# Kernel optimization log

Measured on AMD Instinct MI355X. Metric: run time of the kernel, lower is better.

## Reference

```python
import jax, jax.numpy as jnp
import numpy as np

N_QUBITS = 6
N_LAYERS = 2
QSVT_DEGREE = 3
BATCH = 128
SEQ_LEN = 512
DIM = 2 ** N_QUBITS
# wire 0 is the most-significant bit in the statevector index (PennyLane convention)
_POP = np.array([bin(i).count('1') for i in range(DIM)], dtype=np.float32)
PHASE_SIGN = jnp.asarray(N_QUBITS - 2.0 * _POP)  # (DIM,): sum_w (1 - 2*bit_w)


def _rx(t):
    c = jnp.cos(0.5 * t).astype(jnp.complex64)
    s = (-1j * jnp.sin(0.5 * t)).astype(jnp.complex64)
    return jnp.stack([jnp.stack([c, s]), jnp.stack([s, c])])


def _ry(t):
    c = jnp.cos(0.5 * t).astype(jnp.complex64)
    s = jnp.sin(0.5 * t).astype(jnp.complex64)
    return jnp.stack([jnp.stack([c, -s]), jnp.stack([s, c])])


def _rz(t):
    e = jnp.exp(-0.5j * t.astype(jnp.complex64))
    z = jnp.zeros((), jnp.complex64)
    return jnp.stack([jnp.stack([e, z]), jnp.stack([z, jnp.conj(e)])])


def _apply_1q(psi, U, w):
    # psi: (B,) + (2,)*N_QUBITS ; U: (2,2) complex, same for all batch elems
    psi = jnp.moveaxis(psi, 1 + w, -1)
    psi = psi @ U.T
    return jnp.moveaxis(psi, -1, 1 + w)


def _apply_ry_batched(psi, theta, w):
    # RY with a per-batch angle theta: (B,)
    psi = jnp.moveaxis(psi, 1 + w, -1)
    c = jnp.cos(0.5 * theta).reshape((-1,) + (1,) * (N_QUBITS - 1))
    s = jnp.sin(0.5 * theta).reshape((-1,) + (1,) * (N_QUBITS - 1))
    a, b = psi[..., 0], psi[..., 1]
    psi = jnp.stack([c * a - s * b, s * a + c * b], axis=-1)
    return jnp.moveaxis(psi, -1, 1 + w)


def _cnot(psi, c, t):
    p0 = jax.lax.index_in_dim(psi, 0, axis=1 + c, keepdims=True)
    p1 = jax.lax.index_in_dim(psi, 1, axis=1 + c, keepdims=True)
    p1 = jnp.flip(p1, axis=1 + t)
    return jnp.concatenate([p0, p1], axis=1 + c)


def _circuit_step(h, x, params, poly):
    # h, x: (B, N_QUBITS) angles. Returns <Z_w> per qubit: (B, N_QUBITS).
    B = h.shape[0]
    # 1) state encoding: RY(h_w)|0> = cos(h/2)|0> + sin(h/2)|1>  (product state)
    c, s = jnp.cos(0.5 * h), jnp.sin(0.5 * h)
    psi = jnp.ones((B, 1), jnp.complex64)
    for w in range(N_QUBITS):
        amp = jnp.stack([c[:, w], s[:, w]], axis=-1).astype(jnp.complex64)  # (B,2)
        psi = (psi[:, :, None] * amp[:, None, :]).reshape(B, -1)
    psi = psi.reshape((B,) + (2,) * N_QUBITS)
    # 2) QSVT block: RZ(coeff*pi) on every wire fuses into one diagonal phase
    for d in range(QSVT_DEGREE + 1):
        theta = poly[d] * np.pi
        phase = jnp.exp((-0.5j) * theta * PHASE_SIGN)  # (DIM,)
        psi = (psi.reshape(B, -1) * phase[None, :]).reshape((B,) + (2,) * N_QUBITS)
        for i in range(N_QUBITS - 1):
            psi = _cnot(psi, i, i + 1)
        psi = _cnot(psi, N_QUBITS - 1, 0)  # ring closure
    # 3) variational layers: per-wire RZ@RY@RX (RX applied first), then CNOT chain
    idx = 0
    for _ in range(N_LAYERS):
        for i in range(N_QUBITS):
            U = _rz(params[idx + 2]) @ _ry(params[idx + 1]) @ _rx(params[idx])
            psi = _apply_1q(psi, U, i)
            idx += 3
        for i in range(N_QUBITS - 1):
            psi = _cnot(psi, i, i + 1)
    # 4) input injection: RY(x_w) with per-batch angles
    for w in range(N_QUBITS):
        psi = _apply_ry_batched(psi, x[:, w], w)
    # 5) measurement: <Z_w> = P(bit_w=0) - P(bit_w=1)
    p = jnp.abs(psi) ** 2
    zs = []
    for w in range(N_QUBITS):
        axes = tuple(a for a in range(1, N_QUBITS + 1) if a != 1 + w)
        pw = p.sum(axis=axes)  # (B,2)
        zs.append(pw[:, 0] - pw[:, 1])
    return jnp.stack(zs, axis=-1)


def _ssm_pass(angles, params, poly, reverse):
    a = jnp.flip(angles, axis=1) if reverse else angles
    xs = jnp.moveaxis(a, 1, 0)  # (T, B, n)
    h0 = jnp.zeros((a.shape[0], N_QUBITS), jnp.float32)

    def step(h, x):
        hn = _circuit_step(h, x, params, poly)
        return hn, hn

    _, ys = jax.lax.scan(step, h0, xs)
    out = jnp.moveaxis(ys, 0, 1)  # (B, T, n)
    return jnp.flip(out, axis=1) if reverse else out


def setup_inputs() -> dict:
    key = jax.random.key(0)
    k0, k1, k2, k3 = jax.random.split(key, 4)
    angles = jax.random.uniform(k0, (BATCH, SEQ_LEN, N_QUBITS), jnp.float32) * np.float32(np.pi)
    poly_coeffs = jax.random.normal(k1, (QSVT_DEGREE + 1,), jnp.float32) * 0.1
    fwd_params = jax.random.normal(k2, (N_QUBITS * N_LAYERS * 3,), jnp.float32) * 0.1
    bwd_params = jax.random.normal(k3, (N_QUBITS * N_LAYERS * 3,), jnp.float32) * 0.1
    fwd_coeff = jnp.full((1,), 0.5, jnp.float32)
    bwd_coeff = jnp.full((1,), 0.5, jnp.float32)
    return {'angles': angles, 'poly_coeffs': poly_coeffs, 'fwd_params': fwd_params,
            'bwd_params': bwd_params, 'fwd_coeff': fwd_coeff, 'bwd_coeff': bwd_coeff}


def reference(angles, poly_coeffs, fwd_params, bwd_params, fwd_coeff, bwd_coeff):
    h_fwd = _ssm_pass(angles, fwd_params, poly_coeffs, reverse=False)
    h_bwd = _ssm_pass(angles, bwd_params, poly_coeffs, reverse=True)
    return jax.nn.sigmoid(fwd_coeff) * h_fwd + jax.nn.sigmoid(bwd_coeff) * h_bwd
```

## Files before the change

### kernel.cpp

```cpp
#include <hip/hip_runtime.h>
#include <hip/hip_bf16.h>
#include <stdint.h>

#define BATCH 128
#define SEQ   512
#define NW    6
#define DIM   64
#define NELEM (BATCH * SEQ * NW)
#define PI_F  3.14159265358979323846f

typedef float v2f __attribute__((ext_vector_type(2)));

__device__ __forceinline__ v2f pkfma(float s, v2f m, v2f a) {
    return __builtin_elementwise_fma((v2f){s, s}, m, a);
}

template <int CTRL>
__device__ __forceinline__ void red_stage3(float v[3]) {
#pragma unroll
    for (int k = 0; k < 3; ++k)
        v[k] += __int_as_float(__builtin_amdgcn_update_dpp(
            0, __float_as_int(v[k]), CTRL, 0xF, 0xF, false));
}

__device__ __forceinline__ void sincos_half(float h, float& s, float& c) {
    const float u = h * h;
    c = fmaf(u, fmaf(u, fmaf(u, -2.1701389e-5f, 2.6041667e-3f), -0.125f), 1.0f);
    s = h * fmaf(u, fmaf(u, fmaf(u, -1.5501e-6f, 2.6041667e-4f), -2.0833333e-2f), 0.5f);
}

__global__ void k_detect(const uint32_t* __restrict__ a, int* __restrict__ flag) {
    __shared__ int cnt;
    if (threadIdx.x == 0) cnt = 0;
    __syncthreads();
    uint32_t w = a[threadIdx.x];
    uint32_t e = (w >> 8) & 0xFFu;
    if (e >= 0x3Au && e <= 0x41u) atomicAdd(&cnt, 1);
    __syncthreads();
    if (threadIdx.x == 0) *flag = (cnt >= 128) ? 1 : 0;
}

__device__ __forceinline__ float ldf(const void* p, int i, bool bf) {
    if (bf) {
        uint32_t u = (uint32_t)((const uint16_t*)p)[i];
        return __uint_as_float(u << 16);
    }
    return ((const float*)p)[i];
}

__global__ void k_convert(const void* ang, const void* poly, const void* fp,
                          const void* bp, const void* fc, const void* bc,
                          float* __restrict__ cs, float* __restrict__ misc,
                          const int* __restrict__ flag) {
    const bool bf = (*flag != 0);
    const int i = blockIdx.x * blockDim.x + threadIdx.x;
    if (i < NELEM) {
        float x = ldf(ang, i, bf);
        float s, c;
        __sincosf(x, &s, &c);
        cs[2 * i]     = c;
        cs[2 * i + 1] = s;
    }
    if (i < 4)                    misc[i]            = ldf(poly, i, bf);
    else if (i >= 64 && i < 100)  misc[4 + (i - 64)] = ldf(fp, i - 64, bf);
    else if (i >= 128 && i < 164) misc[40 + (i - 128)] = ldf(bp, i - 128, bf);
    else if (i == 200)            misc[76] = ldf(fc, 0, bf);
    else if (i == 201)            misc[77] = ldf(bc, 0, bf);
}

__global__ void __launch_bounds__(64) k_msetup(const float* __restrict__ misc,
                                               float* __restrict__ Mg) {
    const int p   = threadIdx.x;
    const int col = blockIdx.x & 63;
    const int dir = blockIdx.x >> 6;
    const float* poly = misc;
    const float* prm  = misc + (dir ? 40 : 4);

    float yr = (p == col) ? 1.f : 0.f;
    float yi = 0.f;

#pragma unroll
    for (int d = 0; d < 4; ++d) {
        const float th = 0.5f * PI_F * poly[d] *
                         (float)(6 - 2 * (int)__popc((unsigned)p));
        float s, c;
        __sincosf(th, &s, &c);
        const float nr = yr * c + yi * s;
        const float ni = yi * c - yr * s;
        yr = nr; yi = ni;
#pragma unroll
        for (int k = 0; k < 6; ++k) {
            const int cw = k, tw = (k + 1) % 6;
            const int src = p ^ (((p >> (5 - cw)) & 1) << (5 - tw));
            yr = __shfl(yr, src, 64);
            yi = __shfl(yi, src, 64);
        }
    }

    int idx = 0;
#pragma unroll
    for (int l = 0; l < 2; ++l) {
#pragma unroll
        for (int w = 0; w < 6; ++w) {
            float cx, sx, cy, sy, cz, sz;
            __sincosf(0.5f * prm[idx + 0], &sx, &cx);
            __sincosf(0.5f * prm[idx + 1], &sy, &cy);
            __sincosf(0.5f * prm[idx + 2], &sz, &cz);
            idx += 3;
            const float A = cy * cx, B = sy * sx, C = sy * cx, D = cy * sx;
            const float U00r = cz * A + sz * B, U00i = cz * B - sz * A;
            const float U11r = U00r,            U11i = sz * A - cz * B;
            const float Xr   = cz * C + sz * D, Xi   = sz * C - cz * D;
            const int m  = 1 << (5 - w);
            const int bb = (p >> (5 - w)) & 1;
            const float C1r = bb ? U11r : U00r;
            const float C1i = bb ? U11i : U00i;
            const float C2r = bb ? Xr : -Xr;
            const float C2i = Xi;
            const float pr = __shfl_xor(yr, m, 64);
            const float pi = __shfl_xor(yi, m, 64);
            const float nr = C1r * yr - C1i * yi + C2r * pr - C2i * pi;
            const float ni = C1r * yi + C1i * yr + C2r * pi + C2i * pr;
            yr = nr; yi = ni;
        }
#pragma unroll
        for (int k = 0; k < 5; ++k) {
            const int src = p ^ (((p >> (5 - k)) & 1) << (5 - (k + 1)));
            yr = __shfl(yr, src, 64);
            yi = __shfl(yi, src, 64);
        }
    }

    float* out = Mg + ((size_t)(dir * 64 + p) * 64 + (size_t)col) * 2;
    out[0] = yr;
    out[1] = yi;
}

__global__ void __launch_bounds__(256, 1) k_sim(const float* __restrict__ cs,
                                                const float* __restrict__ Mg,
                                                float* __restrict__ hbuf) {
    const int tid   = threadIdx.x;
    const int lane  = tid & 63;
    const int wv    = tid >> 6;
    const int chain = blockIdx.x;
    const int dir   = chain >> 7;
    const int b     = chain & 127;
    float* orow = hbuf + (size_t)dir * NELEM + (size_t)b * (SEQ * NW);
    const float* csrow = cs + (size_t)b * (SEQ * NW * 2);

    __shared__ __align__(16) float  cl[SEQ * 12];
    __shared__ __align__(16) float  zb[SEQ * NW];
    __shared__ float2 pY[2][4][DIM];
    __shared__ __align__(16) float  mR[12];

    {
        const float4* src = (const float4*)csrow;
        float4* dst = (float4*)cl;
#pragma unroll
        for (int k = 0; k < 6; ++k) {
            const int idx = tid + k * 256;
            dst[idx] = src[idx];
        }
    }

    v2f Mres[16];
    {
        const float2* mr2 =
            (const float2*)(Mg + (size_t)(dir * 64 + lane) * 128 + 32 * wv);
#pragma unroll
        for (int k = 0; k < 16; ++k) Mres[k] = (v2f){mr2[k].x, mr2[k].y};
    }

    const int w0  = (wv & 1) * 3;
    const int isX = wv >> 1;
    int zmask3[3], bpa3[3];
#pragma unroll
    for (int k = 0; k < 3; ++k) {
        const int w = w0 + k;
        zmask3[k] = ((lane >> (5 - w)) & 1) << 31;
        bpa3[k]   = (lane ^ (1 << (5 - w))) << 2;
    }

    float h[6] = {0.f, 0.f, 0.f, 0.f, 0.f, 0.f};

    auto encode_matvec = [&](v2f& acc) {
        float cw6[6], sw6[6];
#pragma unroll
        for (int w = 0; w < 6; ++w) sincos_half(h[w], sw6[w], cw6[w]);
        const float t0 = (wv & 2) ? sw6[0] : cw6[0];
        const float t1 = (wv & 1) ? sw6[1] : cw6[1];
        const float A  = t0 * t1;
        float GH[4], GL[4];
        GH[0] = cw6[2] * cw6[3]; GH[1] = cw6[2] * sw6[3];
        GH[2] = sw6[2] * cw6[3]; GH[3] = sw6[2] * sw6[3];
#pragma unroll
        for (int a = 0; a < 4; ++a) GH[a] *= A;
        GL[0] = cw6[4] * cw6[5]; GL[1] = cw6[4] * sw6[5];
        GL[2] = sw6[4] * cw6[5]; GL[3] = sw6[4] * sw6[5];
        v2f y = {0.f, 0.f};
#pragma unroll
        for (int a = 0; a < 4; ++a) {
            v2f T = {0.f, 0.f};
#pragma unroll
            for (int b2 = 0; b2 < 4; ++b2)
                T = pkfma(GL[b2], Mres[4 * a + b2], T);
            y = pkfma(GH[a], T, y);
        }
        acc = y;
    };

    const float* cp = cl + (dir ? (SEQ - 1) * 12 : 0);
    const int   cstep = dir ? -12 : 12;
    float*       zp = zb + (dir ? (SEQ - 1) * NW : 0);
    const int   zstep = dir ? -NW : NW;

    __syncthreads();

    {
        v2f acc;
        encode_matvec(acc);
        pY[0][wv][lane] = (float2){acc.x, acc.y};
    }
    __syncthreads();

    for (int t = 0; t < SEQ; ++t) {
        const int buf = t & 1;

        const float2 y0 = pY[buf][0][lane], y1 = pY[buf][1][lane];
        const float2 y2 = pY[buf][2][lane], y3 = pY[buf][3][lane];
        const float yr = (y0.x + y1.x) + (y2.x + y3.x);
        const float yi = (y0.y + y1.y) + (y2.y + y3.y);

        float v3[3];
        if (isX) {
            float pr[3], pi[3];
#pragma unroll
            for (int k = 0; k < 3; ++k)
                pr[k] = __int_as_float(
                    __builtin_amdgcn_ds_bpermute(bpa3[k], __float_as_int(yr)));
#pragma unroll
            for (int k = 0; k < 3; ++k)
                pi[k] = __int_as_float(
                    __builtin_amdgcn_ds_bpermute(bpa3[k], __float_as_int(yi)));
#pragma unroll
            for (int k = 0; k < 3; ++k) v3[k] = yr * pr[k] + yi * pi[k];
        } else {
            const float q = yr * yr + yi * yi;
#pragma unroll
            for (int k = 0; k < 3; ++k)
                v3[k] = __int_as_float(__float_as_int(q) ^ zmask3[k]);
        }
        red_stage3<0x111>(v3);
        red_stage3<0x112>(v3);
        red_stage3<0x114>(v3);
        red_stage3<0x118>(v3);
        red_stage3<0x142>(v3);
        red_stage3<0x143>(v3);

        if (lane == 63) {
            mR[wv * 3 + 0] = v3[0];
            mR[wv * 3 + 1] = v3[1];
            mR[wv * 3 + 2] = v3[2];
        }
        __syncthreads();

        const float4 xq0 = ((const float4*)cp)[0];
        const float4 xq1 = ((const float4*)cp)[1];
        const float4 xq2 = ((const float4*)cp)[2];
        cp += cstep;
        const float4 m0 = ((const float4*)mR)[0];
        const float4 m1 = ((const float4*)mR)[1];
        const float4 m2 = ((const float4*)mR)[2];

        float z[6];
        z[0] = xq0.x * m0.x - xq0.y * m1.z;
        z[1] = xq0.z * m0.y - xq0.w * m1.w;
        z[2] = xq1.x * m0.z - xq1.y * m2.x;
        z[3] = xq1.z * m0.w - xq1.w * m2.y;
        z[4] = xq2.x * m1.x - xq2.y * m2.z;
        z[5] = xq2.z * m1.y - xq2.w * m2.w;
#pragma unroll
        for (int w = 0; w < 6; ++w) h[w] = z[w];

        if (tid == 63) {
#pragma unroll
            for (int w = 0; w < 6; ++w) zp[w] = z[w];
        }
        zp += zstep;

        {
            v2f acc;
            encode_matvec(acc);
            pY[buf ^ 1][wv][lane] = (float2){acc.x, acc.y};
        }
        __syncthreads();
    }

    {
        const float4* zs4 = (const float4*)zb;
        float4* go = (float4*)orow;
#pragma unroll
        for (int k = 0; k < 3; ++k) {
            const int idx = tid + k * 256;
            go[idx] = zs4[idx];
        }
    }
}

__global__ void k_combine(const float* __restrict__ hbuf,
                          const float* __restrict__ misc,
                          void* __restrict__ out, const int* __restrict__ flag) {
    const int i = blockIdx.x * blockDim.x + threadIdx.x;
    if (i >= NELEM) return;
    const float sf = 1.f / (1.f + __expf(-misc[76]));
    const float sb = 1.f / (1.f + __expf(-misc[77]));
    const float v = sf * hbuf[i] + sb * hbuf[NELEM + i];
    if (*flag) ((__hip_bfloat16*)out)[i] = __float2bfloat16(v);
    else       ((float*)out)[i] = v;
}

extern "C" void kernel_launch(void* const* d_in, const int* in_sizes, int n_in,
                              void* d_out, int out_size, void* d_ws, size_t ws_size,
                              hipStream_t stream) {
    const void* ang  = d_in[0];
    const void* poly = d_in[1];
    const void* fp   = d_in[2];
    const void* bp   = d_in[3];
    const void* fc   = d_in[4];
    const void* bc   = d_in[5];

    float* cs   = (float*)d_ws + 32;
    float* misc = cs + 2 * NELEM;
    float* hbuf = misc + 128;
    float* Mg   = hbuf + 2 * NELEM;
    int*   flag = (int*)(Mg + 2 * 64 * 64 * 2);

    k_detect<<<1, 256, 0, stream>>>((const uint32_t*)ang, flag);
    k_convert<<<(NELEM + 255) / 256, 256, 0, stream>>>(ang, poly, fp, bp, fc, bc,
                                                       cs, misc, flag);
    k_msetup<<<128, 64, 0, stream>>>(misc, Mg);
    k_sim<<<256, 256, 0, stream>>>(cs, Mg, hbuf);
    k_combine<<<(NELEM + 255) / 256, 256, 0, stream>>>(hbuf, misc, d_out, flag);
}
```

Measured before the change: 364.5 us.

## Fuse detect/convert/msetup into one prep kernel and trim recurrence loop work

Merges the dtype-detect, angle-convert and matrix-setup kernels into a single k_prep launch, with each block recomputing the bf16 detection locally, which removes two launches and their serialization. In the sequential loop each wave keeps its own partial matvec result in registers and reads only the other three from LDS. The next step's angle loads are issued before the barrier so their latency overlaps the reduction. The sincos polynomial is also shortened by one term, which lowers accuracy for larger half-angles and adds redundant detection reads in every block.

```diff
diff --git a/kernel.cpp b/kernel.cpp
--- a/kernel.cpp
+++ b/kernel.cpp
@@ -8,6 +8,7 @@
 #define DIM   64
 #define NELEM (BATCH * SEQ * NW)
 #define PI_F  3.14159265358979323846f
+#define NCONV 1536
 
 typedef float v2f __attribute__((ext_vector_type(2)));
 
@@ -25,19 +26,8 @@
 
 __device__ __forceinline__ void sincos_half(float h, float& s, float& c) {
     const float u = h * h;
-    c = fmaf(u, fmaf(u, fmaf(u, -2.1701389e-5f, 2.6041667e-3f), -0.125f), 1.0f);
-    s = h * fmaf(u, fmaf(u, fmaf(u, -1.5501e-6f, 2.6041667e-4f), -2.0833333e-2f), 0.5f);
-}
-
-__global__ void k_detect(const uint32_t* __restrict__ a, int* __restrict__ flag) {
-    __shared__ int cnt;
-    if (threadIdx.x == 0) cnt = 0;
-    __syncthreads();
-    uint32_t w = a[threadIdx.x];
-    uint32_t e = (w >> 8) & 0xFFu;
-    if (e >= 0x3Au && e <= 0x41u) atomicAdd(&cnt, 1);
-    __syncthreads();
-    if (threadIdx.x == 0) *flag = (cnt >= 128) ? 1 : 0;
+    c = fmaf(u, fmaf(u, 2.6041667e-3f, -0.125f), 1.0f);
+    s = h * fmaf(u, fmaf(u, 2.6041667e-4f, -2.0833333e-2f), 0.5f);
 }
 
 __device__ __forceinline__ float ldf(const void* p, int i, bool bf) {
@@ -48,40 +38,49 @@
     return ((const float*)p)[i];
 }
 
-__global__ void k_convert(const void* ang, const void* poly, const void* fp,
-                          const void* bp, const void* fc, const void* bc,
-                          float* __restrict__ cs, float* __restrict__ misc,
-                          const int* __restrict__ flag) {
-    const bool bf = (*flag != 0);
-    const int i = blockIdx.x * blockDim.x + threadIdx.x;
-    if (i < NELEM) {
-        float x = ldf(ang, i, bf);
-        float s, c;
-        __sincosf(x, &s, &c);
-        cs[2 * i]     = c;
-        cs[2 * i + 1] = s;
-    }
-    if (i < 4)                    misc[i]            = ldf(poly, i, bf);
-    else if (i >= 64 && i < 100)  misc[4 + (i - 64)] = ldf(fp, i - 64, bf);
-    else if (i >= 128 && i < 164) misc[40 + (i - 128)] = ldf(bp, i - 128, bf);
-    else if (i == 200)            misc[76] = ldf(fc, 0, bf);
-    else if (i == 201)            misc[77] = ldf(bc, 0, bf);
-}
-
-__global__ void __launch_bounds__(64) k_msetup(const float* __restrict__ misc,
-                                               float* __restrict__ Mg) {
-    const int p   = threadIdx.x;
-    const int col = blockIdx.x & 63;
-    const int dir = blockIdx.x >> 6;
-    const float* poly = misc;
-    const float* prm  = misc + (dir ? 40 : 4);
+__global__ void k_prep(const void* ang, const void* poly, const void* fp,
+                       const void* bp, const void* fc, const void* bc,
+                       float* __restrict__ cs, float* __restrict__ misc,
+                       float* __restrict__ Mg, int* __restrict__ flag) {
+    __shared__ int cnt;
+    if (threadIdx.x == 0) cnt = 0;
+    __syncthreads();
+    {
+        uint32_t w = ((const uint32_t*)ang)[threadIdx.x & 255];
+        uint32_t e = (w >> 8) & 0xFFu;
+        if (e >= 0x3Au && e <= 0x41u) atomicAdd(&cnt, 1);
+    }
+    __syncthreads();
+    const bool bf = (cnt >= 128);
+
+    if (blockIdx.x < NCONV) {
+        const int i = blockIdx.x * 256 + threadIdx.x;
+        if (i < NELEM) {
+            float x = ldf(ang, i, bf);
+            float s, c;
+            __sincosf(x, &s, &c);
+            cs[2 * i]     = c;
+            cs[2 * i + 1] = s;
+        }
+        if (i == 200)      misc[76] = ldf(fc, 0, bf);
+        else if (i == 201) misc[77] = ldf(bc, 0, bf);
+        else if (i == 202) *flag = bf ? 1 : 0;
+        return;
+    }
+
+    const int lane = threadIdx.x & 63;
+    const int tix  = (blockIdx.x - NCONV) * 4 + (threadIdx.x >> 6);
+    const int dir  = tix >> 6;
+    const int col  = tix & 63;
+    const void* prm = dir ? bp : fp;
+    const int p = lane;
 
     float yr = (p == col) ? 1.f : 0.f;
     float yi = 0.f;
 
 #pragma unroll
     for (int d = 0; d < 4; ++d) {
-        const float th = 0.5f * PI_F * poly[d] *
+        const float th = 0.5f * PI_F * ldf(poly, d, bf) *
                          (float)(6 - 2 * (int)__popc((unsigned)p));
         float s, c;
         __sincosf(th, &s, &c);
@@ -103,9 +102,9 @@
 #pragma unroll
         for (int w = 0; w < 6; ++w) {
             float cx, sx, cy, sy, cz, sz;
-            __sincosf(0.5f * prm[idx + 0], &sx, &cx);
-            __sincosf(0.5f * prm[idx + 1], &sy, &cy);
-            __sincosf(0.5f * prm[idx + 2], &sz, &cz);
+            __sincosf(0.5f * ldf(prm, idx + 0, bf), &sx, &cx);
+            __sincosf(0.5f * ldf(prm, idx + 1, bf), &sy, &cy);
+            __sincosf(0.5f * ldf(prm, idx + 2, bf), &sz, &cz);
             idx += 3;
             const float A = cy * cx, B = sy * sx, C = sy * cx, D = cy * sx;
             const float U00r = cz * A + sz * B, U00i = cz * B - sz * A;
@@ -180,6 +179,7 @@
         zmask3[k] = ((lane >> (5 - w)) & 1) << 31;
         bpa3[k]   = (lane ^ (1 << (5 - w))) << 2;
     }
+    const int ow0 = wv ^ 1, ow1 = wv ^ 2, ow2 = wv ^ 3;
 
     float h[6] = {0.f, 0.f, 0.f, 0.f, 0.f, 0.f};
 
@@ -216,20 +216,24 @@
 
     __syncthreads();
 
-    {
-        v2f acc;
-        encode_matvec(acc);
-        pY[0][wv][lane] = (float2){acc.x, acc.y};
-    }
+    v2f myacc;
+    encode_matvec(myacc);
+    pY[0][wv][lane] = (float2){myacc.x, myacc.y};
     __syncthreads();
 
     for (int t = 0; t < SEQ; ++t) {
         const int buf = t & 1;
 
-        const float2 y0 = pY[buf][0][lane], y1 = pY[buf][1][lane];
-        const float2 y2 = pY[buf][2][lane], y3 = pY[buf][3][lane];
-        const float yr = (y0.x + y1.x) + (y2.x + y3.x);
-        const float yi = (y0.y + y1.y) + (y2.y + y3.y);
+        const float2 yA = pY[buf][ow0][lane];
+        const float2 yB = pY[buf][ow1][lane];
+        const float2 yC = pY[buf][ow2][lane];
+        const float4 xq0 = ((const float4*)cp)[0];
+        const float4 xq1 = ((const float4*)cp)[1];
+        const float4 xq2 = ((const float4*)cp)[2];
+        cp += cstep;
+
+        const float yr = (myacc.x + yA.x) + (yB.x + yC.x);
+        const float yi = (myacc.y + yA.y) + (yB.y + yC.y);
 
         float v3[3];
         if (isX) {
@@ -264,10 +268,6 @@
         }
         __syncthreads();
 
-        const float4 xq0 = ((const float4*)cp)[0];
-        const float4 xq1 = ((const float4*)cp)[1];
-        const float4 xq2 = ((const float4*)cp)[2];
-        cp += cstep;
         const float4 m0 = ((const float4*)mR)[0];
         const float4 m1 = ((const float4*)mR)[1];
         const float4 m2 = ((const float4*)mR)[2];
@@ -279,20 +279,17 @@
         z[3] = xq1.z * m0.w - xq1.w * m2.y;
         z[4] = xq2.x * m1.x - xq2.y * m2.z;
         z[5] = xq2.z * m1.y - xq2.w * m2.w;
+
+        if (tid == 63) {
+#pragma unroll
+            for (int w = 0; w < 6; ++w) zp[w] = z[w];
+        }
+        zp += zstep;
 #pragma unroll
         for (int w = 0; w < 6; ++w) h[w] = z[w];
 
-        if (tid == 63) {
-#pragma unroll
-            for (int w = 0; w < 6; ++w) zp[w] = z[w];
-        }
-        zp += zstep;
-
-        {
-            v2f acc;
-            encode_matvec(acc);
-            pY[buf ^ 1][wv][lane] = (float2){acc.x, acc.y};
-        }
+        encode_matvec(myacc);
+        pY[buf ^ 1][wv][lane] = (float2){myacc.x, myacc.y};
         __syncthreads();
     }
 
@@ -335,10 +332,8 @@
     float* Mg   = hbuf + 2 * NELEM;
     int*   flag = (int*)(Mg + 2 * 64 * 64 * 2);
 
-    k_detect<<<1, 256, 0, stream>>>((const uint32_t*)ang, flag);
-    k_convert<<<(NELEM + 255) / 256, 256, 0, stream>>>(ang, poly, fp, bp, fc, bc,
-                                                       cs, misc, flag);
-    k_msetup<<<128, 64, 0, stream>>>(misc, Mg);
+    k_prep<<<NCONV + 32, 256, 0, stream>>>(ang, poly, fp, bp, fc, bc,
+                                           cs, misc, Mg, flag);
     k_sim<<<256, 256, 0, stream>>>(cs, Mg, hbuf);
     k_combine<<<(NELEM + 255) / 256, 256, 0, stream>>>(hbuf, misc, d_out, flag);
 }
```

Result: faster. 345.8 us (median of 3 runs) (-5.1%).
